# Kernel optimization log

Hardware: AMD Instinct MI355X
Metric: run time of the kernel (lower is better)

Reference implementation:

```python
import jax, jax.numpy as jnp
import numpy as np

B, S, HIST = 2, 2048, 2048
H, HK, D = 16, 16, 128
DIM = H * D

def setup_inputs() -> dict:
    key = jax.random.key(0)
    ks = jax.random.split(key, 8)
    x = jax.random.normal(ks[0], (B, S, DIM), jnp.float32)
    prev_k = jax.random.normal(ks[1], (B, HIST, HK, D), jnp.float32)
    prev_v = jax.random.normal(ks[2], (B, HIST, HK, D), jnp.float32)
    # causal mask: history fully visible, causal within the current chunk
    q_pos = HIST + jnp.arange(S)
    k_pos = jnp.arange(HIST + S)
    mask = jnp.where(k_pos[None, :] <= q_pos[:, None], 0.0, -1e9).astype(jnp.float32)[None, None]
    sc = 0.02
    wq = jax.random.normal(ks[3], (DIM, DIM), jnp.float32) * sc
    wk = jax.random.normal(ks[4], (DIM, DIM), jnp.float32) * sc
    wv = jax.random.normal(ks[5], (DIM, DIM), jnp.float32) * sc
    wo = jax.random.normal(ks[6], (DIM, DIM), jnp.float32) * sc
    return {"x": x, "prev_k": prev_k, "prev_v": prev_v, "mask": mask,
            "wq": wq, "wk": wk, "wv": wv, "wo": wo}

def reference(x, prev_k, prev_v, mask, wq, wk, wv, wo):
    b, s, _ = x.shape
    # nn.Linear: y = x @ W^T, weights stored [out, in]
    xq = jnp.einsum('bsd,ed->bse', x, wq).reshape(b, s, H, D)
    xk = jnp.einsum('bsd,ed->bse', x, wk).reshape(b, s, HK, D)
    xv = jnp.einsum('bsd,ed->bse', x, wv).reshape(b, s, HK, D)
    k_all = jnp.concatenate([prev_k, xk], axis=1)  # [b, hist+s, hk, d]
    v_all = jnp.concatenate([prev_v, xv], axis=1)
    scores = jnp.einsum('bqhd,bkhd->bhqk', xq, k_all) / jnp.sqrt(jnp.float32(D))
    scores = scores + mask
    probs = jax.nn.softmax(scores.astype(jnp.float32), axis=-1).astype(xq.dtype)
    out = jnp.einsum('bhqk,bkhd->bqhd', probs, v_all).reshape(b, s, H * D)
    out = jnp.einsum('bse,de->bsd', out, wo)
    return out, k_all, v_all
```

## Files before the change

kernel.cpp:

```cpp
#include <hip/hip_runtime.h>
#include <math.h>

typedef __attribute__((ext_vector_type(8))) short bf16x8;
typedef __attribute__((ext_vector_type(4))) short bf16x4;
typedef __attribute__((ext_vector_type(4))) float f32x4;

#define SSCL (0.08838834764831845f * 1.4426950408889634f)

__device__ __forceinline__ short f2bf(float f) {
    union { float f; unsigned u; } x; x.f = f;
    unsigned r = x.u + 0x7fffu + ((x.u >> 16) & 1u);
    return (short)(r >> 16);
}
__device__ __forceinline__ float bf2f(short s) {
    union { unsigned u; float f; } x;
    x.u = ((unsigned)(unsigned short)s) << 16;
    return x.f;
}

typedef const __attribute__((address_space(1))) unsigned int* gas_ptr;
typedef __attribute__((address_space(3))) unsigned int* las_ptr;
__device__ __forceinline__ void async_copy16(const void* g, void* l) {
    __builtin_amdgcn_global_load_lds((gas_ptr)g, (las_ptr)l, 16, 0, 0);
}

__global__ __launch_bounds__(256)
void cvt_kernel(const float* __restrict__ src, short* __restrict__ dst, int n4) {
    int i = blockIdx.x * 256 + threadIdx.x;
    const int stride = gridDim.x * 256;
    for (; i < n4; i += stride) {
        float4 v = ((const float4*)src)[i];
        bf16x4 o;
        o[0] = f2bf(v.x); o[1] = f2bf(v.y); o[2] = f2bf(v.z); o[3] = f2bf(v.w);
        ((bf16x4*)dst)[i] = o;
    }
}

template<int QKV>
__global__ __launch_bounds__(256)
void gemm_kernel(const short* __restrict__ A,
                 const short* __restrict__ B0, const short* __restrict__ B1,
                 const short* __restrict__ B2,
                 short* __restrict__ D16, float* __restrict__ Dk,
                 float* __restrict__ Dv, float* __restrict__ Df) {
    __shared__ short As[128 * 64];
    __shared__ short Bs[128 * 64];
    const int tid = threadIdx.x, w = tid >> 6, ln = tid & 63;
    const int col = ln & 15, quad = ln >> 4;
    const int sel = QKV ? (blockIdx.x >> 4) : 0;
    const int tn = (blockIdx.x & 15) * 128;
    const int tm = blockIdx.y * 128;
    const short* B = (sel == 0) ? B0 : ((sel == 1) ? B1 : B2);

    const int wm = (w >> 1) * 64, wn = (w & 1) * 64;
    const int srow = ln >> 3, scol = (ln & 7) * 8;

    f32x4 acc[4][4];
    for (int i = 0; i < 4; ++i)
        for (int j = 0; j < 4; ++j)
            for (int e = 0; e < 4; ++e) acc[i][j][e] = 0.f;

    for (int k0 = 0; k0 < 2048; k0 += 64) {
        #pragma unroll
        for (int i = 0; i < 4; ++i) {
            int chunk = i * 4 + w;
            int row = chunk * 8 + srow;
            async_copy16(&A[(tm + row) * 2048 + k0 + scol], &As[chunk * 512]);
            async_copy16(&B[(tn + row) * 2048 + k0 + scol], &Bs[chunk * 512]);
        }
        asm volatile("s_waitcnt vmcnt(0)" ::: "memory");
        __syncthreads();
        #pragma unroll
        for (int kk = 0; kk < 2; ++kk) {
            bf16x8 af[4], bfr[4];
            #pragma unroll
            for (int i = 0; i < 4; ++i)
                af[i] = *(const bf16x8*)&As[(wm + i * 16 + col) * 64 + kk * 32 + quad * 8];
            #pragma unroll
            for (int j = 0; j < 4; ++j)
                bfr[j] = *(const bf16x8*)&Bs[(wn + j * 16 + col) * 64 + kk * 32 + quad * 8];
            __builtin_amdgcn_s_setprio(1);
            #pragma unroll
            for (int i = 0; i < 4; ++i)
                #pragma unroll
                for (int j = 0; j < 4; ++j)
                    acc[i][j] = __builtin_amdgcn_mfma_f32_16x16x32_bf16(af[i], bfr[j], acc[i][j], 0, 0, 0);
            __builtin_amdgcn_s_setprio(0);
        }
        __syncthreads();
    }
    for (int i = 0; i < 4; ++i)
        for (int j = 0; j < 4; ++j)
            for (int r = 0; r < 4; ++r) {
                int m = tm + wm + i * 16 + quad * 4 + r;
                int n = tn + wn + j * 16 + col;
                float v = acc[i][j][r];
                if (QKV) {
                    if (sel == 0) {
                        D16[m * 2048 + n] = f2bf(v);
                    } else {
                        int orow = m + ((m >> 11) + 1) * 2048;
                        float* D = (sel == 1) ? Dk : Dv;
                        D[orow * 2048 + n] = v;
                    }
                } else {
                    Df[m * 2048 + n] = v;
                }
            }
}

__global__ __launch_bounds__(256)
void prep_v(const float* __restrict__ Vall, short* __restrict__ Vtg) {
    __shared__ short L[64 * 132];
    const int tid = threadIdx.x;
    const int k0 = blockIdx.x * 64;
    const int h = blockIdx.y, b = blockIdx.z;
    const float* Vb = Vall + ((size_t)(b * 4096) * 16 + h) * 128;
    short* Vo = Vtg + ((size_t)(b * 16 + h) * 128) * 4096;
    #pragma unroll
    for (int i = 0; i < 8; ++i) {
        int idx = i * 256 + tid;
        int r = idx >> 5, c4 = (idx & 31) * 4;
        float4 v = *(const float4*)&Vb[(size_t)(k0 + r) * 2048 + c4];
        bf16x4 o4;
        o4[0] = f2bf(v.x); o4[1] = f2bf(v.y); o4[2] = f2bf(v.z); o4[3] = f2bf(v.w);
        *(bf16x4*)&L[r * 132 + c4] = o4;
    }
    __syncthreads();
    #pragma unroll
    for (int i = 0; i < 8; ++i) {
        int idx = i * 256 + tid;
        int d = idx >> 4, kc4 = (idx & 15) * 4;
        bf16x4 o4;
        o4[0] = L[(kc4 + 0) * 132 + d];
        o4[1] = L[(kc4 + 1) * 132 + d];
        o4[2] = L[(kc4 + 2) * 132 + d];
        o4[3] = L[(kc4 + 3) * 132 + d];
        *(bf16x4*)&Vo[(size_t)d * 4096 + k0 + (kc4 ^ ((d & 7) << 3))] = o4;
    }
}

__global__ __launch_bounds__(256)
void attn_mfma(const short* __restrict__ Q, const float* __restrict__ Kall,
               const short* __restrict__ Vtg, short* __restrict__ Ot) {
    __shared__ short Ks[64 * 128];
    __shared__ short Vs[128 * 64];
    __shared__ short Ps[4 * 16 * 72];
    const int tid = threadIdx.x, w = tid >> 6, ln = tid & 63;
    const int col = ln & 15, quad = ln >> 4;
    const int s0 = blockIdx.x * 64;
    const int h = blockIdx.y, b = blockIdx.z;
    const int xk = (col & 7) << 3;

    bf16x8 qf[4];
    {
        const int qr = (b * 2048 + s0 + w * 16 + col) * 2048 + h * 128;
        #pragma unroll
        for (int ks = 0; ks < 4; ++ks)
            qf[ks] = *(const bf16x8*)&Q[qr + ks * 32 + quad * 8];
    }
    f32x4 o[8];
    #pragma unroll
    for (int i = 0; i < 8; ++i)
        for (int e = 0; e < 4; ++e) o[i][e] = 0.f;
    float mr[4] = {-1e30f, -1e30f, -1e30f, -1e30f};
    float lr[4] = {0.f, 0.f, 0.f, 0.f};

    const float* Kb = Kall + ((size_t)(b * 4096) * 16 + h) * 128;
    const short* Vb = Vtg + ((size_t)(b * 16 + h) * 128) * 4096;
    short* PsW = &Ps[w * 1152];

    const int vd = (ln >> 3);
    const int vkofs = (ln & 7) * 8;
    const int kr0 = tid >> 5;
    const int kc4 = (tid & 31) * 4;
    const int kswz = (kc4 ^ ((kr0 & 7) << 3));

    const int ntiles = 33 + blockIdx.x;
    for (int t = 0; t < ntiles; ++t) {
        const int k0 = t * 64;
        #pragma unroll
        for (int i = 0; i < 4; ++i) {
            int ch = i * 4 + w;
            async_copy16(&Vb[(size_t)(ch * 8 + vd) * 4096 + k0 + vkofs], &Vs[ch * 512]);
        }
        #pragma unroll
        for (int i = 0; i < 8; ++i) {
            int kr = i * 8 + kr0;
            float4 kv = *(const float4*)&Kb[(size_t)(k0 + kr) * 2048 + kc4];
            bf16x4 kb4;
            kb4[0] = f2bf(kv.x); kb4[1] = f2bf(kv.y);
            kb4[2] = f2bf(kv.z); kb4[3] = f2bf(kv.w);
            *(bf16x4*)&Ks[kr * 128 + kswz] = kb4;
        }
        asm volatile("s_waitcnt vmcnt(0)" ::: "memory");
        __syncthreads();

        f32x4 s4[4];
        #pragma unroll
        for (int j = 0; j < 4; ++j)
            for (int e = 0; e < 4; ++e) s4[j][e] = 0.f;
        #pragma unroll
        for (int ks = 0; ks < 4; ++ks) {
            const int dofs = (ks * 32 + quad * 8) ^ xk;
            bf16x8 kf[4];
            #pragma unroll
            for (int j = 0; j < 4; ++j)
                kf[j] = *(const bf16x8*)&Ks[(j * 16 + col) * 128 + dofs];
            __builtin_amdgcn_s_setprio(1);
            #pragma unroll
            for (int j = 0; j < 4; ++j)
                s4[j] = __builtin_amdgcn_mfma_f32_16x16x32_bf16(qf[ks], kf[j], s4[j], 0, 0, 0);
            __builtin_amdgcn_s_setprio(0);
        }
        const bool full = (k0 + 63 <= 2048 + s0 + w * 16);
        float p[4][4];
        if (full) {
            #pragma unroll
            for (int j = 0; j < 4; ++j)
                #pragma unroll
                for (int r = 0; r < 4; ++r) p[j][r] = s4[j][r] * SSCL;
        } else {
            #pragma unroll
            for (int j = 0; j < 4; ++j) {
                int kp = k0 + j * 16 + col;
                #pragma unroll
                for (int r = 0; r < 4; ++r) {
                    int qp = 2048 + s0 + w * 16 + quad * 4 + r;
                    p[j][r] = (kp <= qp) ? s4[j][r] * SSCL : -1e30f;
                }
            }
        }
        #pragma unroll
        for (int r = 0; r < 4; ++r) {
            float mx = fmaxf(fmaxf(p[0][r], p[1][r]), fmaxf(p[2][r], p[3][r]));
            mx = fmaxf(mx, __shfl_xor(mx, 1));
            mx = fmaxf(mx, __shfl_xor(mx, 2));
            mx = fmaxf(mx, __shfl_xor(mx, 4));
            mx = fmaxf(mx, __shfl_xor(mx, 8));
            float mn = fmaxf(mr[r], mx);
            float al = exp2f(mr[r] - mn);
            mr[r] = mn;
            float rs = 0.f;
            #pragma unroll
            for (int j = 0; j < 4; ++j) { p[j][r] = exp2f(p[j][r] - mn); rs += p[j][r]; }
            rs += __shfl_xor(rs, 1);
            rs += __shfl_xor(rs, 2);
            rs += __shfl_xor(rs, 4);
            rs += __shfl_xor(rs, 8);
            lr[r] = lr[r] * al + rs;
            #pragma unroll
            for (int i = 0; i < 8; ++i) o[i][r] *= al;
        }
        #pragma unroll
        for (int j = 0; j < 4; ++j)
            #pragma unroll
            for (int r = 0; r < 4; ++r)
                PsW[(quad * 4 + r) * 72 + j * 16 + col] = f2bf(p[j][r]);
        bf16x8 pa0 = *(const bf16x8*)&PsW[col * 72 + quad * 8];
        bf16x8 pa1 = *(const bf16x8*)&PsW[col * 72 + 32 + quad * 8];
        #pragma unroll
        for (int dt = 0; dt < 8; ++dt) {
            int row = dt * 16 + col;
            bf16x8 v0 = *(const bf16x8*)&Vs[row * 64 + ((quad * 8) ^ xk)];
            bf16x8 v1 = *(const bf16x8*)&Vs[row * 64 + ((32 + quad * 8) ^ xk)];
            __builtin_amdgcn_s_setprio(1);
            o[dt] = __builtin_amdgcn_mfma_f32_16x16x32_bf16(pa0, v0, o[dt], 0, 0, 0);
            o[dt] = __builtin_amdgcn_mfma_f32_16x16x32_bf16(pa1, v1, o[dt], 0, 0, 0);
            __builtin_amdgcn_s_setprio(0);
        }
        __syncthreads();
    }
    const int orow = (b * 2048 + s0 + w * 16) * 2048 + h * 128;
    #pragma unroll
    for (int r = 0; r < 4; ++r) {
        float inv = 1.f / lr[r];
        #pragma unroll
        for (int dt = 0; dt < 8; ++dt)
            Ot[orow + (quad * 4 + r) * 2048 + dt * 16 + col] = f2bf(o[dt][r] * inv);
    }
}

extern "C" void kernel_launch(void* const* d_in, const int* in_sizes, int n_in,
                              void* d_out, int out_size, void* d_ws, size_t ws_size,
                              hipStream_t stream) {
    const float* x  = (const float*)d_in[0];
    const float* pk = (const float*)d_in[1];
    const float* pv = (const float*)d_in[2];
    const float* wq = (const float*)d_in[4];
    const float* wk = (const float*)d_in[5];
    const float* wv = (const float*)d_in[6];
    const float* wo = (const float*)d_in[7];

    float* out  = (float*)d_out;
    float* kall = out + 8388608;
    float* vall = out + 25165824;

    short* ws16 = (short*)d_ws;
    short* xb  = ws16;
    short* wqb = ws16 + 8388608;
    short* wkb = ws16 + 12582912;
    short* wvb = ws16 + 16777216;
    short* wob = ws16 + 20971520;
    short* vtg = ws16 + 8388608;
    short* qbf = ws16 + 25165824;
    short* ot  = xb;

    hipMemcpyAsync(kall,           pk,           16777216u, hipMemcpyDeviceToDevice, stream);
    hipMemcpyAsync(kall + 8388608, pk + 4194304, 16777216u, hipMemcpyDeviceToDevice, stream);
    hipMemcpyAsync(vall,           pv,           16777216u, hipMemcpyDeviceToDevice, stream);
    hipMemcpyAsync(vall + 8388608, pv + 4194304, 16777216u, hipMemcpyDeviceToDevice, stream);

    cvt_kernel<<<1024, 256, 0, stream>>>(x,  xb,  2097152);
    cvt_kernel<<<512,  256, 0, stream>>>(wq, wqb, 1048576);
    cvt_kernel<<<512,  256, 0, stream>>>(wk, wkb, 1048576);
    cvt_kernel<<<512,  256, 0, stream>>>(wv, wvb, 1048576);

    gemm_kernel<1><<<dim3(48, 32), 256, 0, stream>>>(xb, wqb, wkb, wvb,
                                                     qbf, kall, vall, nullptr);
    prep_v<<<dim3(64, 16, 2), 256, 0, stream>>>(vall, vtg);
    attn_mfma<<<dim3(32, 16, 2), 256, 0, stream>>>(qbf, kall, vtg, ot);
    cvt_kernel<<<512, 256, 0, stream>>>(wo, wob, 1048576);
    gemm_kernel<0><<<dim3(16, 32), 256, 0, stream>>>(ot, wob, wob, wob,
                                                     nullptr, nullptr, nullptr, out);
}
```

Measured before the change: 929.6 us.

## Process two 64-row query tiles per attention block to reuse K/V tiles

Each attention workgroup now handles 128 query rows (two 64-row fragments per wave) instead of 64. Every K and V tile staged in LDS, including the per-tile fp32-to-bf16 conversion of K, is therefore shared by twice as many queries, roughly halving global K/V traffic and conversion work. The grid is re-indexed so batch and head map to blockIdx.x and the query tile to blockIdx.y, and a skip flag avoids softmax and PV work on the first fragment for fully masked tiles. The cost is more registers per thread (two sets of accumulators and Q fragments), which may lower occupancy, and half as many blocks, which may worsen load balance across the causal triangle.

```diff
diff --git a/kernel.cpp b/kernel.cpp
--- a/kernel.cpp
+++ b/kernel.cpp
@@ -145,30 +145,38 @@
                const short* __restrict__ Vtg, short* __restrict__ Ot) {
     __shared__ short Ks[64 * 128];
     __shared__ short Vs[128 * 64];
-    __shared__ short Ps[4 * 16 * 72];
+    __shared__ short Ps[2 * 4 * 16 * 72];
     const int tid = threadIdx.x, w = tid >> 6, ln = tid & 63;
     const int col = ln & 15, quad = ln >> 4;
-    const int s0 = blockIdx.x * 64;
-    const int h = blockIdx.y, b = blockIdx.z;
+    const int bh = blockIdx.x;
+    const int b = bh >> 4, h = bh & 15;
+    const int s0 = blockIdx.y * 128;
     const int xk = (col & 7) << 3;
 
-    bf16x8 qf[4];
-    {
-        const int qr = (b * 2048 + s0 + w * 16 + col) * 2048 + h * 128;
+    bf16x8 qf[2][4];
+    #pragma unroll
+    for (int f = 0; f < 2; ++f) {
+        const int qr = (b * 2048 + s0 + f * 64 + w * 16 + col) * 2048 + h * 128;
         #pragma unroll
         for (int ks = 0; ks < 4; ++ks)
-            qf[ks] = *(const bf16x8*)&Q[qr + ks * 32 + quad * 8];
-    }
-    f32x4 o[8];
-    #pragma unroll
-    for (int i = 0; i < 8; ++i)
-        for (int e = 0; e < 4; ++e) o[i][e] = 0.f;
-    float mr[4] = {-1e30f, -1e30f, -1e30f, -1e30f};
-    float lr[4] = {0.f, 0.f, 0.f, 0.f};
+            qf[f][ks] = *(const bf16x8*)&Q[qr + ks * 32 + quad * 8];
+    }
+    f32x4 o[2][8];
+    #pragma unroll
+    for (int f = 0; f < 2; ++f)
+        #pragma unroll
+        for (int i = 0; i < 8; ++i)
+            for (int e = 0; e < 4; ++e) o[f][i][e] = 0.f;
+    float mr[2][4], lr[2][4];
+    #pragma unroll
+    for (int f = 0; f < 2; ++f)
+        #pragma unroll
+        for (int r = 0; r < 4; ++r) { mr[f][r] = -1e30f; lr[f][r] = 0.f; }
 
     const float* Kb = Kall + ((size_t)(b * 4096) * 16 + h) * 128;
     const short* Vb = Vtg + ((size_t)(b * 16 + h) * 128) * 4096;
-    short* PsW = &Ps[w * 1152];
+    short* P0w = &Ps[w * 1152];
+    short* P1w = &Ps[4608 + w * 1152];
 
     const int vd = (ln >> 3);
     const int vkofs = (ln & 7) * 8;
@@ -176,7 +184,7 @@
     const int kc4 = (tid & 31) * 4;
     const int kswz = (kc4 ^ ((kr0 & 7) << 3));
 
-    const int ntiles = 33 + blockIdx.x;
+    const int ntiles = 34 + 2 * blockIdx.y;
     for (int t = 0; t < ntiles; ++t) {
         const int k0 = t * 64;
         #pragma unroll
@@ -196,10 +204,14 @@
         asm volatile("s_waitcnt vmcnt(0)" ::: "memory");
         __syncthreads();
 
-        f32x4 s4[4];
-        #pragma unroll
-        for (int j = 0; j < 4; ++j)
-            for (int e = 0; e < 4; ++e) s4[j][e] = 0.f;
+        const bool act0 = (k0 <= 2048 + s0 + w * 16 + 15);
+
+        f32x4 s4[2][4];
+        #pragma unroll
+        for (int f = 0; f < 2; ++f)
+            #pragma unroll
+            for (int j = 0; j < 4; ++j)
+                for (int e = 0; e < 4; ++e) s4[f][j][e] = 0.f;
         #pragma unroll
         for (int ks = 0; ks < 4; ++ks) {
             const int dofs = (ks * 32 + quad * 8) ^ xk;
@@ -210,74 +222,94 @@
             __builtin_amdgcn_s_setprio(1);
             #pragma unroll
             for (int j = 0; j < 4; ++j)
-                s4[j] = __builtin_amdgcn_mfma_f32_16x16x32_bf16(qf[ks], kf[j], s4[j], 0, 0, 0);
+                s4[0][j] = __builtin_amdgcn_mfma_f32_16x16x32_bf16(qf[0][ks], kf[j], s4[0][j], 0, 0, 0);
+            #pragma unroll
+            for (int j = 0; j < 4; ++j)
+                s4[1][j] = __builtin_amdgcn_mfma_f32_16x16x32_bf16(qf[1][ks], kf[j], s4[1][j], 0, 0, 0);
             __builtin_amdgcn_s_setprio(0);
         }
-        const bool full = (k0 + 63 <= 2048 + s0 + w * 16);
-        float p[4][4];
-        if (full) {
-            #pragma unroll
-            for (int j = 0; j < 4; ++j)
-                #pragma unroll
-                for (int r = 0; r < 4; ++r) p[j][r] = s4[j][r] * SSCL;
-        } else {
-            #pragma unroll
-            for (int j = 0; j < 4; ++j) {
-                int kp = k0 + j * 16 + col;
-                #pragma unroll
-                for (int r = 0; r < 4; ++r) {
-                    int qp = 2048 + s0 + w * 16 + quad * 4 + r;
-                    p[j][r] = (kp <= qp) ? s4[j][r] * SSCL : -1e30f;
+
+        #pragma unroll
+        for (int f = 0; f < 2; ++f) {
+            if (f == 0 && !act0) continue;
+            const int qbase = 2048 + s0 + f * 64 + w * 16;
+            const bool full = (k0 + 63 <= qbase);
+            float p[4][4];
+            if (full) {
+                #pragma unroll
+                for (int j = 0; j < 4; ++j)
+                    #pragma unroll
+                    for (int r = 0; r < 4; ++r) p[j][r] = s4[f][j][r] * SSCL;
+            } else {
+                #pragma unroll
+                for (int j = 0; j < 4; ++j) {
+                    int kp = k0 + j * 16 + col;
+                    #pragma unroll
+                    for (int r = 0; r < 4; ++r) {
+                        int qp = qbase + quad * 4 + r;
+                        p[j][r] = (kp <= qp) ? s4[f][j][r] * SSCL : -1e30f;
+                    }
                 }
             }
-        }
-        #pragma unroll
-        for (int r = 0; r < 4; ++r) {
-            float mx = fmaxf(fmaxf(p[0][r], p[1][r]), fmaxf(p[2][r], p[3][r]));
-            mx = fmaxf(mx, __shfl_xor(mx, 1));
-            mx = fmaxf(mx, __shfl_xor(mx, 2));
-            mx = fmaxf(mx, __shfl_xor(mx, 4));
-            mx = fmaxf(mx, __shfl_xor(mx, 8));
-            float mn = fmaxf(mr[r], mx);
-            float al = exp2f(mr[r] - mn);
-            mr[r] = mn;
-            float rs = 0.f;
-            #pragma unroll
-            for (int j = 0; j < 4; ++j) { p[j][r] = exp2f(p[j][r] - mn); rs += p[j][r]; }
-            rs += __shfl_xor(rs, 1);
-            rs += __shfl_xor(rs, 2);
-            rs += __shfl_xor(rs, 4);
-            rs += __shfl_xor(rs, 8);
-            lr[r] = lr[r] * al + rs;
-            #pragma unroll
-            for (int i = 0; i < 8; ++i) o[i][r] *= al;
-        }
-        #pragma unroll
-        for (int j = 0; j < 4; ++j)
-            #pragma unroll
-            for (int r = 0; r < 4; ++r)
-                PsW[(quad * 4 + r) * 72 + j * 16 + col] = f2bf(p[j][r]);
-        bf16x8 pa0 = *(const bf16x8*)&PsW[col * 72 + quad * 8];
-        bf16x8 pa1 = *(const bf16x8*)&PsW[col * 72 + 32 + quad * 8];
+            #pragma unroll
+            for (int r = 0; r < 4; ++r) {
+                float mx = fmaxf(fmaxf(p[0][r], p[1][r]), fmaxf(p[2][r], p[3][r]));
+                mx = fmaxf(mx, __shfl_xor(mx, 1));
+                mx = fmaxf(mx, __shfl_xor(mx, 2));
+                mx = fmaxf(mx, __shfl_xor(mx, 4));
+                mx = fmaxf(mx, __shfl_xor(mx, 8));
+                float mn = fmaxf(mr[f][r], mx);
+                float al = exp2f(mr[f][r] - mn);
+                mr[f][r] = mn;
+                float rs = 0.f;
+                #pragma unroll
+                for (int j = 0; j < 4; ++j) { p[j][r] = exp2f(p[j][r] - mn); rs += p[j][r]; }
+                rs += __shfl_xor(rs, 1);
+                rs += __shfl_xor(rs, 2);
+                rs += __shfl_xor(rs, 4);
+                rs += __shfl_xor(rs, 8);
+                lr[f][r] = lr[f][r] * al + rs;
+                #pragma unroll
+                for (int i = 0; i < 8; ++i) o[f][i][r] *= al;
+            }
+            short* Pf = (f == 0) ? P0w : P1w;
+            #pragma unroll
+            for (int j = 0; j < 4; ++j)
+                #pragma unroll
+                for (int r = 0; r < 4; ++r)
+                    Pf[(quad * 4 + r) * 72 + j * 16 + col] = f2bf(p[j][r]);
+        }
+
+        bf16x8 pa00 = *(const bf16x8*)&P0w[col * 72 + quad * 8];
+        bf16x8 pa01 = *(const bf16x8*)&P0w[col * 72 + 32 + quad * 8];
+        bf16x8 pa10 = *(const bf16x8*)&P1w[col * 72 + quad * 8];
+        bf16x8 pa11 = *(const bf16x8*)&P1w[col * 72 + 32 + quad * 8];
         #pragma unroll
         for (int dt = 0; dt < 8; ++dt) {
             int row = dt * 16 + col;
             bf16x8 v0 = *(const bf16x8*)&Vs[row * 64 + ((quad * 8) ^ xk)];
             bf16x8 v1 = *(const bf16x8*)&Vs[row * 64 + ((32 + quad * 8) ^ xk)];
             __builtin_amdgcn_s_setprio(1);
-            o[dt] = __builtin_amdgcn_mfma_f32_16x16x32_bf16(pa0, v0, o[dt], 0, 0, 0);
-            o[dt] = __builtin_amdgcn_mfma_f32_16x16x32_bf16(pa1, v1, o[dt], 0, 0, 0);
+            if (act0) {
+                o[0][dt] = __builtin_amdgcn_mfma_f32_16x16x32_bf16(pa00, v0, o[0][dt], 0, 0, 0);
+                o[0][dt] = __builtin_amdgcn_mfma_f32_16x16x32_bf16(pa01, v1, o[0][dt], 0, 0, 0);
+            }
+            o[1][dt] = __builtin_amdgcn_mfma_f32_16x16x32_bf16(pa10, v0, o[1][dt], 0, 0, 0);
+            o[1][dt] = __builtin_amdgcn_mfma_f32_16x16x32_bf16(pa11, v1, o[1][dt], 0, 0, 0);
             __builtin_amdgcn_s_setprio(0);
         }
         __syncthreads();
     }
-    const int orow = (b * 2048 + s0 + w * 16) * 2048 + h * 128;
-    #pragma unroll
-    for (int r = 0; r < 4; ++r) {
-        float inv = 1.f / lr[r];
-        #pragma unroll
-        for (int dt = 0; dt < 8; ++dt)
-            Ot[orow + (quad * 4 + r) * 2048 + dt * 16 + col] = f2bf(o[dt][r] * inv);
+    #pragma unroll
+    for (int f = 0; f < 2; ++f) {
+        const int orow = (b * 2048 + s0 + f * 64 + w * 16) * 2048 + h * 128;
+        #pragma unroll
+        for (int r = 0; r < 4; ++r) {
+            float inv = 1.f / lr[f][r];
+            #pragma unroll
+            for (int dt = 0; dt < 8; ++dt)
+                Ot[orow + (quad * 4 + r) * 2048 + dt * 16 + col] = f2bf(o[f][dt][r] * inv);
+        }
     }
 }
 
@@ -319,7 +351,7 @@
     gemm_kernel<1><<<dim3(48, 32), 256, 0, stream>>>(xb, wqb, wkb, wvb,
                                                      qbf, kall, vall, nullptr);
     prep_v<<<dim3(64, 16, 2), 256, 0, stream>>>(vall, vtg);
-    attn_mfma<<<dim3(32, 16, 2), 256, 0, stream>>>(qbf, kall, vtg, ot);
+    attn_mfma<<<dim3(32, 16), 256, 0, stream>>>(qbf, kall, vtg, ot);
     cvt_kernel<<<512, 256, 0, stream>>>(wo, wob, 1048576);
     gemm_kernel<0><<<dim3(16, 32), 256, 0, stream>>>(ot, wob, wob, wob,
                                                      nullptr, nullptr, nullptr, out);
```

New measurement: 1.165 ms. +25.3%, slower.

## Double-buffer K/V tiles in attention and remap grid so batch-head is fastest

Applied to the files above, without the earlier changes.

The attention kernel now keeps two LDS buffers for K and V. It issues the next tile's global loads (K into registers, V via async LDS copy) before computing the current tile, then converts K to bf16 and stores it after the PV MFMAs, which removes the load-then-wait stall at the top of each iteration. The grid is also remapped so batch*head varies along blockIdx.x and the sequence block along y, which changes dispatch order and how the causal-length imbalance is spread across CUs. In exchange, LDS use doubles and K prefetch holds 8 float4 registers live, which may reduce occupancy.

```diff
diff --git a/kernel.cpp b/kernel.cpp
--- a/kernel.cpp
+++ b/kernel.cpp
@@ -143,13 +143,14 @@
 __global__ __launch_bounds__(256)
 void attn_mfma(const short* __restrict__ Q, const float* __restrict__ Kall,
                const short* __restrict__ Vtg, short* __restrict__ Ot) {
-    __shared__ short Ks[64 * 128];
-    __shared__ short Vs[128 * 64];
+    __shared__ short Ks[2][64 * 128];
+    __shared__ short Vs[2][128 * 64];
     __shared__ short Ps[4 * 16 * 72];
     const int tid = threadIdx.x, w = tid >> 6, ln = tid & 63;
     const int col = ln & 15, quad = ln >> 4;
-    const int s0 = blockIdx.x * 64;
-    const int h = blockIdx.y, b = blockIdx.z;
+    const int bh = blockIdx.x;
+    const int b = bh >> 4, h = bh & 15;
+    const int s0 = blockIdx.y * 64;
     const int xk = (col & 7) << 3;
 
     bf16x8 qf[4];
@@ -176,25 +177,45 @@
     const int kc4 = (tid & 31) * 4;
     const int kswz = (kc4 ^ ((kr0 & 7) << 3));
 
-    const int ntiles = 33 + blockIdx.x;
+    const int ntiles = 33 + blockIdx.y;
+
+    float4 kvr[8];
+
+    #pragma unroll
+    for (int i = 0; i < 8; ++i)
+        kvr[i] = *(const float4*)&Kb[(size_t)(i * 8 + kr0) * 2048 + kc4];
+    #pragma unroll
+    for (int i = 0; i < 4; ++i) {
+        int ch = i * 4 + w;
+        async_copy16(&Vb[(size_t)(ch * 8 + vd) * 4096 + vkofs], &Vs[0][ch * 512]);
+    }
+    #pragma unroll
+    for (int i = 0; i < 8; ++i) {
+        bf16x4 kb4;
+        kb4[0] = f2bf(kvr[i].x); kb4[1] = f2bf(kvr[i].y);
+        kb4[2] = f2bf(kvr[i].z); kb4[3] = f2bf(kvr[i].w);
+        *(bf16x4*)&Ks[0][(i * 8 + kr0) * 128 + kswz] = kb4;
+    }
+    asm volatile("s_waitcnt vmcnt(0)" ::: "memory");
+    __syncthreads();
+
     for (int t = 0; t < ntiles; ++t) {
+        const int p = t & 1;
         const int k0 = t * 64;
-        #pragma unroll
-        for (int i = 0; i < 4; ++i) {
-            int ch = i * 4 + w;
-            async_copy16(&Vb[(size_t)(ch * 8 + vd) * 4096 + k0 + vkofs], &Vs[ch * 512]);
-        }
-        #pragma unroll
-        for (int i = 0; i < 8; ++i) {
-            int kr = i * 8 + kr0;
-            float4 kv = *(const float4*)&Kb[(size_t)(k0 + kr) * 2048 + kc4];
-            bf16x4 kb4;
-            kb4[0] = f2bf(kv.x); kb4[1] = f2bf(kv.y);
-            kb4[2] = f2bf(kv.z); kb4[3] = f2bf(kv.w);
-            *(bf16x4*)&Ks[kr * 128 + kswz] = kb4;
-        }
-        asm volatile("s_waitcnt vmcnt(0)" ::: "memory");
-        __syncthreads();
+        const bool pf = (t + 1 < ntiles);
+
+        if (pf) {
+            const int k0n = k0 + 64;
+            #pragma unroll
+            for (int i = 0; i < 8; ++i)
+                kvr[i] = *(const float4*)&Kb[(size_t)(k0n + i * 8 + kr0) * 2048 + kc4];
+            #pragma unroll
+            for (int i = 0; i < 4; ++i) {
+                int ch = i * 4 + w;
+                async_copy16(&Vb[(size_t)(ch * 8 + vd) * 4096 + k0n + vkofs],
+                             &Vs[p ^ 1][ch * 512]);
+            }
+        }
 
         f32x4 s4[4];
         #pragma unroll
@@ -206,20 +227,21 @@
             bf16x8 kf[4];
             #pragma unroll
             for (int j = 0; j < 4; ++j)
-                kf[j] = *(const bf16x8*)&Ks[(j * 16 + col) * 128 + dofs];
+                kf[j] = *(const bf16x8*)&Ks[p][(j * 16 + col) * 128 + dofs];
             __builtin_amdgcn_s_setprio(1);
             #pragma unroll
             for (int j = 0; j < 4; ++j)
                 s4[j] = __builtin_amdgcn_mfma_f32_16x16x32_bf16(qf[ks], kf[j], s4[j], 0, 0, 0);
             __builtin_amdgcn_s_setprio(0);
         }
+
         const bool full = (k0 + 63 <= 2048 + s0 + w * 16);
-        float p[4][4];
+        float pp[4][4];
         if (full) {
             #pragma unroll
             for (int j = 0; j < 4; ++j)
                 #pragma unroll
-                for (int r = 0; r < 4; ++r) p[j][r] = s4[j][r] * SSCL;
+                for (int r = 0; r < 4; ++r) pp[j][r] = s4[j][r] * SSCL;
         } else {
             #pragma unroll
             for (int j = 0; j < 4; ++j) {
@@ -227,13 +249,13 @@
                 #pragma unroll
                 for (int r = 0; r < 4; ++r) {
                     int qp = 2048 + s0 + w * 16 + quad * 4 + r;
-                    p[j][r] = (kp <= qp) ? s4[j][r] * SSCL : -1e30f;
+                    pp[j][r] = (kp <= qp) ? s4[j][r] * SSCL : -1e30f;
                 }
             }
         }
         #pragma unroll
         for (int r = 0; r < 4; ++r) {
-            float mx = fmaxf(fmaxf(p[0][r], p[1][r]), fmaxf(p[2][r], p[3][r]));
+            float mx = fmaxf(fmaxf(pp[0][r], pp[1][r]), fmaxf(pp[2][r], pp[3][r]));
             mx = fmaxf(mx, __shfl_xor(mx, 1));
             mx = fmaxf(mx, __shfl_xor(mx, 2));
             mx = fmaxf(mx, __shfl_xor(mx, 4));
@@ -243,7 +265,7 @@
             mr[r] = mn;
             float rs = 0.f;
             #pragma unroll
-            for (int j = 0; j < 4; ++j) { p[j][r] = exp2f(p[j][r] - mn); rs += p[j][r]; }
+            for (int j = 0; j < 4; ++j) { pp[j][r] = exp2f(pp[j][r] - mn); rs += pp[j][r]; }
             rs += __shfl_xor(rs, 1);
             rs += __shfl_xor(rs, 2);
             rs += __shfl_xor(rs, 4);
@@ -256,19 +278,30 @@
         for (int j = 0; j < 4; ++j)
             #pragma unroll
             for (int r = 0; r < 4; ++r)
-                PsW[(quad * 4 + r) * 72 + j * 16 + col] = f2bf(p[j][r]);
+                PsW[(quad * 4 + r) * 72 + j * 16 + col] = f2bf(pp[j][r]);
         bf16x8 pa0 = *(const bf16x8*)&PsW[col * 72 + quad * 8];
         bf16x8 pa1 = *(const bf16x8*)&PsW[col * 72 + 32 + quad * 8];
         #pragma unroll
         for (int dt = 0; dt < 8; ++dt) {
             int row = dt * 16 + col;
-            bf16x8 v0 = *(const bf16x8*)&Vs[row * 64 + ((quad * 8) ^ xk)];
-            bf16x8 v1 = *(const bf16x8*)&Vs[row * 64 + ((32 + quad * 8) ^ xk)];
+            bf16x8 v0 = *(const bf16x8*)&Vs[p][row * 64 + ((quad * 8) ^ xk)];
+            bf16x8 v1 = *(const bf16x8*)&Vs[p][row * 64 + ((32 + quad * 8) ^ xk)];
             __builtin_amdgcn_s_setprio(1);
             o[dt] = __builtin_amdgcn_mfma_f32_16x16x32_bf16(pa0, v0, o[dt], 0, 0, 0);
             o[dt] = __builtin_amdgcn_mfma_f32_16x16x32_bf16(pa1, v1, o[dt], 0, 0, 0);
             __builtin_amdgcn_s_setprio(0);
         }
+
+        if (pf) {
+            #pragma unroll
+            for (int i = 0; i < 8; ++i) {
+                bf16x4 kb4;
+                kb4[0] = f2bf(kvr[i].x); kb4[1] = f2bf(kvr[i].y);
+                kb4[2] = f2bf(kvr[i].z); kb4[3] = f2bf(kvr[i].w);
+                *(bf16x4*)&Ks[p ^ 1][(i * 8 + kr0) * 128 + kswz] = kb4;
+            }
+        }
+        asm volatile("s_waitcnt vmcnt(0)" ::: "memory");
         __syncthreads();
     }
     const int orow = (b * 2048 + s0 + w * 16) * 2048 + h * 128;
@@ -319,7 +352,7 @@
     gemm_kernel<1><<<dim3(48, 32), 256, 0, stream>>>(xb, wqb, wkb, wvb,
                                                      qbf, kall, vall, nullptr);
     prep_v<<<dim3(64, 16, 2), 256, 0, stream>>>(vall, vtg);
-    attn_mfma<<<dim3(32, 16, 2), 256, 0, stream>>>(qbf, kall, vtg, ot);
+    attn_mfma<<<dim3(32, 32), 256, 0, stream>>>(qbf, kall, vtg, ot);
     cvt_kernel<<<512, 256, 0, stream>>>(wo, wob, 1048576);
     gemm_kernel<0><<<dim3(16, 32), 256, 0, stream>>>(ot, wob, wob, wob,
                                                      nullptr, nullptr, nullptr, out);
```

Measured after the change: 858.3 us. 1.08x faster.
